# Optimization experiments

Measured on AMD Instinct MI355X. Metric: run time of the kernel, lower is better.

Reference implementation:

```python
import jax, jax.numpy as jnp
import numpy as np
from jax import lax

# dims
B, T, C, V, L = 4, 1024, 1024, 32000, 2
NR, NT, E = 6, 2, 8          # rwkv experts, transformer experts, total
HID = 4 * C                  # FFN hidden
P, R = 8, 64                 # bridge prefix_len, low_rank_dim
NH, HD = 16, 64              # heads, head_size


def _layernorm(x, g, b, eps=1e-5):
    m = jnp.mean(x, axis=-1, keepdims=True)
    v = jnp.var(x, axis=-1, keepdims=True)
    return (x - m) * lax.rsqrt(v + eps) * g + b


def setup_inputs() -> dict:
    key = jax.random.key(0)
    ks = list(jax.random.split(key, 32))
    it = iter(ks)
    def nrm(shape, s=0.02):
        return jax.random.normal(next(it), shape, dtype=jnp.float32) * s
    inp = {}
    inp['idx'] = jax.random.randint(next(it), (B, T), 0, V)
    inp['capital_shares'] = jax.random.uniform(next(it), (L, E), dtype=jnp.float32)
    inp['emb'] = nrm((V, C), 1.0)
    inp['head'] = nrm((C, V))
    inp['ln1_g'] = jnp.ones((L, C), jnp.float32)
    inp['ln1_b'] = jnp.zeros((L, C), jnp.float32)
    inp['ln2_g'] = jnp.ones((L, C), jnp.float32)
    inp['ln2_b'] = jnp.zeros((L, C), jnp.float32)
    inp['lno_g'] = jnp.ones((C,), jnp.float32)
    inp['lno_b'] = jnp.zeros((C,), jnp.float32)
    inp['att_Wr'] = nrm((L, C, C))
    inp['att_Wk'] = nrm((L, C, C))
    inp['att_Wv'] = nrm((L, C, C))
    inp['att_Wo'] = nrm((L, C, C))
    inp['att_decay'] = nrm((L, C), 1.0)
    inp['critic_wd'] = nrm((L, C))
    inp['critic_Wa'] = nrm((L, C, E))
    inp['bridge_Wdown'] = nrm((C, R))
    inp['bridge_Wup'] = nrm((P, R, C))
    inp['eWk'] = nrm((L, NR, C, HID))
    inp['eWv'] = nrm((L, NR, HID, C))
    inp['conf_r'] = nrm((L, NR, C))
    inp['tWq'] = nrm((L, NT, C, C))
    inp['tWk'] = nrm((L, NT, C, C))
    inp['tWv'] = nrm((L, NT, C, C))
    inp['tWo'] = nrm((L, NT, C, C))
    inp['conf_t'] = nrm((L, NT, C))
    return inp


def _forward(idx, capital_shares, emb, head, ln1_g, ln1_b, ln2_g, ln2_b,
             lno_g, lno_b, att_Wr, att_Wk, att_Wv, att_Wo, att_decay,
             critic_wd, critic_Wa, bridge_Wdown, bridge_Wup,
             eWk, eWv, conf_r, tWq, tWk, tWv, tWo, conf_t):
    x = emb[idx]                                   # [B,T,C]
    v_first = jnp.zeros_like(x)
    for l in range(L):
        # --- TimeMix (simplified RWKV: per-channel decayed kv state) ---
        x_ln = _layernorm(x, ln1_g[l], ln1_b[l])
        r = jax.nn.sigmoid(x_ln @ att_Wr[l])       # [B,T,C]
        k = x_ln @ att_Wk[l]
        v = x_ln @ att_Wv[l]
        if l == 0:
            v_first = v
        else:
            v = 0.5 * (v + v_first)
        w = jax.nn.sigmoid(att_decay[l])           # [C] decay in (0,1)
        def step(s, kv):
            kt, vt = kv
            s = w * s + kt * vt
            return s, s
        kT = jnp.swapaxes(k, 0, 1)                 # [T,B,C]
        vT = jnp.swapaxes(v, 0, 1)
        _, s_seq = lax.scan(step, jnp.zeros((B, C), x.dtype), (kT, vT))
        rwkv_state = jnp.swapaxes(s_seq, 0, 1)     # [B,T,C]
        att_out = (r * rwkv_state) @ att_Wo[l]
        x = x + att_out
        # --- routing (market) ---
        h = _layernorm(x, ln2_g[l], ln2_b[l])
        conf_rw = jax.nn.sigmoid(jnp.einsum('btc,ec->bte', h, conf_r[l]))
        conf_tr = jax.nn.sigmoid(jnp.einsum('btc,ec->bte', h, conf_t[l]))
        confidences = jnp.concatenate([conf_rw, conf_tr], axis=-1)  # [B,T,E]
        difficulty = jax.nn.softplus(jnp.einsum('btc,c->bt', h, critic_wd[l]))[..., None]
        affinity = jnp.einsum('btc,ce->bte', h, critic_Wa[l])
        subsidy = jnp.tanh(affinity)               # critic.apply_to_bids(0, affinity)
        bids = confidences * capital_shares[l] * difficulty + subsidy
        top2_vals, winners = lax.top_k(bids, 2)    # [B,T,2]
        weights = jax.nn.softmax(top2_vals, axis=-1)
        gate = (weights[..., 0:1] * jax.nn.one_hot(winners[..., 0], E, dtype=h.dtype)
                + weights[..., 1:2] * jax.nn.one_hot(winners[..., 1], E, dtype=h.dtype))  # [B,T,E]
        # --- bridge prefix (low-rank, shared) ---
        flat_h = h.reshape(-1, C)
        flat_state = rwkv_state.reshape(-1, C)
        u = (flat_h + flat_state) @ bridge_Wdown   # [N,R]
        prefix = jnp.einsum('nr,prc->npc', u, bridge_Wup)  # [N,P,C]
        # --- experts: dense-equivalent of gather/compute/scatter ---
        final = jnp.zeros_like(h)
        for e in range(NR):                        # squared-relu FFN experts
            hid = jnp.square(jax.nn.relu(h @ eWk[l, e]))
            final = final + gate[..., e:e + 1] * (hid @ eWv[l, e])
        scale = 1.0 / jnp.sqrt(jnp.float32(HD))
        for j in range(NT):                        # linear transformer experts over prefix
            q = (flat_h @ tWq[l, j]).reshape(-1, NH, HD)
            kp = (prefix @ tWk[l, j]).reshape(-1, P, NH, HD)
            vp = (prefix @ tWv[l, j]).reshape(-1, P, NH, HD)
            attn = jax.nn.softmax(jnp.einsum('nhd,nphd->nhp', q, kp) * scale, axis=-1)
            o = jnp.einsum('nhp,nphd->nhd', attn, vp).reshape(-1, C) @ tWo[l, j]
            final = final + gate[..., NR + j:NR + j + 1] * o.reshape(B, T, C)
        x = x + final
    x = _layernorm(x, lno_g, lno_b)
    return x @ head                                # [B,T,V] logits


def reference(idx, capital_shares, emb, head, ln1_g, ln1_b, ln2_g, ln2_b,
              lno_g, lno_b, att_Wr, att_Wk, att_Wv, att_Wo, att_decay,
              critic_wd, critic_Wa, bridge_Wdown, bridge_Wup,
              eWk, eWv, conf_r, tWq, tWk, tWv, tWo, conf_t):
    return _forward(idx, capital_shares, emb, head, ln1_g, ln1_b, ln2_g, ln2_b,
                    lno_g, lno_b, att_Wr, att_Wk, att_Wv, att_Wo, att_decay,
                    critic_wd, critic_Wa, bridge_Wdown, bridge_Wup,
                    eWk, eWv, conf_r, tWq, tWk, tWv, tWo, conf_t)
```

## Files before the change

### kernel.cpp

```cpp
#include <hip/hip_runtime.h>

typedef _Float16 h16;
typedef __attribute__((ext_vector_type(8))) _Float16 h16x8;
typedef __attribute__((ext_vector_type(4))) _Float16 h16x4;
typedef __attribute__((ext_vector_type(4))) float f32x4;

#define DEVFN static __device__ __forceinline__

DEVFN void gl_lds16(const void* g, void* l) {
  __builtin_amdgcn_global_load_lds((const __attribute__((address_space(1))) unsigned int*)g,
                                   (__attribute__((address_space(3))) unsigned int*)l, 16, 0, 0);
}
DEVFN void fsplit(float v, h16& hi, h16& lo) { hi = (h16)v; lo = (h16)(v - (float)hi); }
DEVFN float wred(float v) {
  #pragma unroll
  for (int m = 32; m >= 1; m >>= 1) v += __shfl_xor(v, m, 64);
  return v;
}
DEVFN float sigm(float x) { return 1.0f / (1.0f + expf(-x)); }
DEVFN float softpl(float x) { return fmaxf(x, 0.0f) + log1pf(expf(-fabsf(x))); }

enum { EPI_WRITE = 0, EPI_ADD = 1, EPI_SQRELU = 3, EPI_TSPLIT = 4, EPI_SCATTER = 5 };

template<bool SPLIT, int EPI, int MODE>
__global__ __launch_bounds__(256, 2) void gemm_k(
    const h16* __restrict__ Ah, const h16* __restrict__ Al, long lda, long sAz,
    const h16* __restrict__ Bh, const h16* __restrict__ Bl, long ldb, long sBz,
    float* __restrict__ C, long ldc, long sCz,
    h16* __restrict__ Oh, h16* __restrict__ Ol, long ldo,
    int K, int nmask, const float* __restrict__ rs, int rsStride,
    const int4* __restrict__ meta, int metaStep,
    const int* __restrict__ lists, int listStep,
    const int* __restrict__ mmap)
{
  __shared__ h16 As[(SPLIT ? 2 : 1) * 4096];
  __shared__ h16 Bs[(SPLIT ? 2 : 1) * 4096];
  const int tid = threadIdx.x;
  const int lane = tid & 63, wave = tid >> 6;
  const int wr = wave >> 1, wc = wave & 1;
  const long z = blockIdx.z;
  const long m0 = (long)blockIdx.x * 128, n0 = (long)blockIdx.y * 128;

  int cntv = 0, eIdx = 0, eOff = 0;
  long koff = 0;
  const int* lst = nullptr;
  if (MODE == 1) {
    const int4 mt = meta[z * metaStep];
    if ((int)m0 >= mt.y) return;
    cntv = mt.x; lst = lists + z * listStep;
  } else if (MODE == 2) {
    const int4 mt = meta[0];
    if ((int)m0 >= mt.y) return;
    cntv = mt.x; lst = lists; koff = z * (long)K;
  } else if (MODE == 3 || MODE == 4) {
    if ((int)m0 >= meta[8].x) return;
    eIdx = mmap[blockIdx.x];
    const int4 mt = meta[eIdx];
    cntv = mt.x; eOff = mt.z;
    lst = lists + eIdx * listStep;
    if (MODE == 4) koff = z * (long)K;
  }

  const long zb = (MODE == 3 || MODE == 4) ? (long)eIdx : z;
  const h16* pAh = Ah + z * sAz;
  const h16* pBh = Bh + zb * sBz;
  const h16* pAl = SPLIT ? (Al + z * sAz) : nullptr;
  const h16* pBl = SPLIT ? (Bl + zb * sBz) : nullptr;
  const int rA = wave * 16 + (lane >> 2);
  const int khalf = (lane & 3) * 8;
  long arow0, arow1;
  if (MODE == 1)      { arow0 = lst[m0 + rA]; arow1 = lst[m0 + rA + 64]; }
  else if (MODE == 3) { arow0 = lst[m0 + rA - eOff]; arow1 = lst[m0 + rA + 64 - eOff]; }
  else                { arow0 = m0 + rA; arow1 = arow0 + 64; }
  const long aoff0 = arow0 * lda + khalf + koff;
  const long aoff1 = arow1 * lda + khalf + koff;
  const long boff = (n0 + rA) * ldb + khalf + koff;
  h16* lA = &As[wave * 512];
  h16* lB = &Bs[wave * 512];
  const int fr = lane & 15, fq = lane >> 4;

  const f32x4 zero = {0.f, 0.f, 0.f, 0.f};
  f32x4 acc[4][4];
  #pragma unroll
  for (int m = 0; m < 4; m++)
    #pragma unroll
    for (int n = 0; n < 4; n++) acc[m][n] = zero;

  for (int k0 = 0; k0 < K; k0 += 32) {
    gl_lds16(pAh + aoff0 + k0, lA);
    gl_lds16(pAh + aoff1 + k0, lA + 2048);
    gl_lds16(pBh + boff + k0, lB);
    gl_lds16(pBh + boff + k0 + 64 * ldb, lB + 2048);
    if (SPLIT) {
      gl_lds16(pAl + aoff0 + k0, lA + 4096);
      gl_lds16(pAl + aoff1 + k0, lA + 4096 + 2048);
      gl_lds16(pBl + boff + k0, lB + 4096);
      gl_lds16(pBl + boff + k0 + 64 * ldb, lB + 4096 + 2048);
    }
    __syncthreads();
    h16x8 af[4], bf[4], afl[4], bfl[4];
    #pragma unroll
    for (int m = 0; m < 4; m++) {
      const int r = (wr * 64 + m * 16 + fr) * 32 + fq * 8;
      af[m] = *(const h16x8*)&As[r];
      if (SPLIT) afl[m] = *(const h16x8*)&As[4096 + r];
    }
    #pragma unroll
    for (int n = 0; n < 4; n++) {
      const int r = (wc * 64 + n * 16 + fr) * 32 + fq * 8;
      bf[n] = *(const h16x8*)&Bs[r];
      if (SPLIT) bfl[n] = *(const h16x8*)&Bs[4096 + r];
    }
    #pragma unroll
    for (int m = 0; m < 4; m++)
      #pragma unroll
      for (int n = 0; n < 4; n++) {
        acc[m][n] = __builtin_amdgcn_mfma_f32_16x16x32_f16(af[m], bf[n], acc[m][n], 0, 0, 0);
        if (SPLIT) {
          acc[m][n] = __builtin_amdgcn_mfma_f32_16x16x32_f16(af[m], bfl[n], acc[m][n], 0, 0, 0);
          acc[m][n] = __builtin_amdgcn_mfma_f32_16x16x32_f16(afl[m], bf[n], acc[m][n], 0, 0, 0);
        }
      }
    __syncthreads();
  }

  #pragma unroll
  for (int m = 0; m < 4; m++) {
    const long lrow = m0 + wr * 64 + m * 16 + fq * 4;
    #pragma unroll
    for (int n = 0; n < 4; n++) {
      const long gcol = n0 + wc * 64 + n * 16 + fr;
      if (nmask && gcol >= nmask) continue;
      if (EPI == EPI_TSPLIT) {
        h16x4 hv, lv;
        #pragma unroll
        for (int i = 0; i < 4; i++) { h16 a, b2; fsplit(acc[m][n][i], a, b2); hv[i] = a; lv[i] = b2; }
        *(h16x4*)&Oh[gcol * ldo + lrow] = hv;
        *(h16x4*)&Ol[gcol * ldo + lrow] = lv;
      } else if (EPI == EPI_SQRELU) {
        #pragma unroll
        for (int i = 0; i < 4; i++) {
          float v = acc[m][n][i];
          v = v > 0.f ? v * v : 0.f;
          const h16 a = (h16)v;
          Oh[(lrow + i) * ldo + gcol] = a;
          if (Ol) Ol[(lrow + i) * ldo + gcol] = (h16)(v - (float)a);
        }
      } else if (EPI == EPI_SCATTER) {
        #pragma unroll
        for (int i = 0; i < 4; i++) {
          const int slot = (int)lrow + i - eOff;
          if (slot >= cntv) continue;
          const int tok = lst[slot];
          const float g = rs[(long)tok * rsStride + (MODE == 4 ? eIdx : 0)];
          atomicAdd(&C[(long)tok * ldc + gcol], g * acc[m][n][i]);
        }
      } else {
        float* cp = C + z * sCz + lrow * ldc + gcol;
        #pragma unroll
        for (int i = 0; i < 4; i++) {
          const float v = acc[m][n][i];
          if (EPI == EPI_WRITE) cp[i * ldc] = v;
          else cp[i * ldc] += v;
        }
      }
    }
  }
}

template<bool LO>
__global__ __launch_bounds__(256) void k_tsplit(
    const float* __restrict__ in, long inZ,
    h16* __restrict__ oh, h16* __restrict__ ol, long outZ, int Kd, int Nd)
{
  __shared__ float t[64][65];
  const long z = blockIdx.z;
  in += z * inZ; oh += z * outZ; if (LO) ol += z * outZ;
  const int n0 = blockIdx.x * 64, k0 = blockIdx.y * 64;
  const int tr = threadIdx.x >> 4, tc = threadIdx.x & 15;
  #pragma unroll
  for (int r = 0; r < 4; r++) {
    const int row = r * 16 + tr;
    const float4 v = *(const float4*)&in[(long)(k0 + row) * Nd + n0 + tc * 4];
    t[row][tc * 4 + 0] = v.x; t[row][tc * 4 + 1] = v.y;
    t[row][tc * 4 + 2] = v.z; t[row][tc * 4 + 3] = v.w;
  }
  __syncthreads();
  #pragma unroll
  for (int r = 0; r < 4; r++) {
    const int nrow = r * 16 + tr;
    h16x4 hv, lv;
    #pragma unroll
    for (int i = 0; i < 4; i++) {
      h16 a, b2; fsplit(t[tc * 4 + i][nrow], a, b2);
      hv[i] = a; lv[i] = b2;
    }
    *(h16x4*)&oh[(long)(n0 + nrow) * Kd + k0 + tc * 4] = hv;
    if (LO) *(h16x4*)&ol[(long)(n0 + nrow) * Kd + k0 + tc * 4] = lv;
  }
}

__global__ void k_split(const float* __restrict__ in, h16* __restrict__ oh, h16* __restrict__ ol)
{
  const long i = (long)blockIdx.x * 256 + threadIdx.x;
  const float4 v = ((const float4*)in)[i];
  h16x4 hv, lv; h16 a, b2;
  fsplit(v.x, a, b2); hv[0] = a; lv[0] = b2;
  fsplit(v.y, a, b2); hv[1] = a; lv[1] = b2;
  fsplit(v.z, a, b2); hv[2] = a; lv[2] = b2;
  fsplit(v.w, a, b2); hv[3] = a; lv[3] = b2;
  ((h16x4*)oh)[i] = hv; ((h16x4*)ol)[i] = lv;
}

__global__ void k_embed(const int* __restrict__ idx, const float* __restrict__ emb, float* __restrict__ x)
{
  const int row = blockIdx.x;
  const long e = (long)idx[row] * 1024;
  ((float4*)(x + (long)row * 1024))[threadIdx.x] = ((const float4*)(emb + e))[threadIdx.x];
}

__global__ __launch_bounds__(256) void k_ln(
    const float* __restrict__ x, const float* __restrict__ g, const float* __restrict__ b,
    float* __restrict__ yf, h16* __restrict__ yh, h16* __restrict__ yl)
{
  const int row = blockIdx.x, tid = threadIdx.x;
  const float4 v = ((const float4*)(x + (long)row * 1024))[tid];
  __shared__ float red[4];
  const int wv = tid >> 6;
  float s = wred(v.x + v.y + v.z + v.w);
  if ((tid & 63) == 0) red[wv] = s;
  __syncthreads();
  const float mean = (red[0] + red[1] + red[2] + red[3]) * (1.0f / 1024.0f);
  const float d0 = v.x - mean, d1 = v.y - mean, d2 = v.z - mean, d3 = v.w - mean;
  float s2 = wred(d0 * d0 + d1 * d1 + d2 * d2 + d3 * d3);
  __syncthreads();
  if ((tid & 63) == 0) red[wv] = s2;
  __syncthreads();
  const float var = (red[0] + red[1] + red[2] + red[3]) * (1.0f / 1024.0f);
  const float rstd = 1.0f / sqrtf(var + 1e-5f);
  const float4 gv = ((const float4*)g)[tid];
  const float4 bv = ((const float4*)b)[tid];
  const float y0 = d0 * rstd * gv.x + bv.x;
  const float y1 = d1 * rstd * gv.y + bv.y;
  const float y2 = d2 * rstd * gv.z + bv.z;
  const float y3 = d3 * rstd * gv.w + bv.w;
  if (yf) { float4 o; o.x = y0; o.y = y1; o.z = y2; o.w = y3; ((float4*)(yf + (long)row * 1024))[tid] = o; }
  h16x4 hv, lv; h16 a, b2;
  fsplit(y0, a, b2); hv[0] = a; lv[0] = b2;
  fsplit(y1, a, b2); hv[1] = a; lv[1] = b2;
  fsplit(y2, a, b2); hv[2] = a; lv[2] = b2;
  fsplit(y3, a, b2); hv[3] = a; lv[3] = b2;
  *(h16x4*)(yh + (long)row * 1024 + tid * 4) = hv;
  if (yl) *(h16x4*)(yl + (long)row * 1024 + tid * 4) = lv;
}

__global__ void k_vfix(float* __restrict__ rkv, float* __restrict__ vfir, int mode)
{
  const int row = blockIdx.x, tid = threadIdx.x;
  float4* vp = (float4*)(rkv + (long)row * 3072 + 2048) + tid;
  float4* fp = (float4*)(vfir + (long)row * 1024) + tid;
  if (mode == 0) *fp = *vp;
  else {
    float4 a = *vp; const float4 b = *fp;
    a.x = 0.5f * (a.x + b.x); a.y = 0.5f * (a.y + b.y);
    a.z = 0.5f * (a.z + b.z); a.w = 0.5f * (a.w + b.w);
    *vp = a;
  }
}

__global__ __launch_bounds__(256) void k_scan1(const float* __restrict__ rkv,
                                               const float* __restrict__ dec, float* __restrict__ carry)
{
  const int gid = blockIdx.x * 256 + threadIdx.x;
  const int c = gid & 1023, bb = (gid >> 10) & 3, ch = gid >> 12;
  const float w = sigm(dec[c]);
  float s = 0.f;
  const long base = ((long)bb * 1024 + ch * 64) * 3072 + c;
  const float* kp_ = rkv + 1024 + base;
  const float* vp_ = rkv + 2048 + base;
  for (int t = 0; t < 64; t++) s = w * s + kp_[(long)t * 3072] * vp_[(long)t * 3072];
  carry[(ch * 4 + bb) * 1024 + c] = s;
}
__global__ void k_scan2(const float* __restrict__ dec, float* __restrict__ carry)
{
  const int gid = blockIdx.x * 256 + threadIdx.x;
  const int c = gid & 1023, bb = gid >> 10;
  const float w = sigm(dec[c]);
  float w64 = w;
  for (int i = 0; i < 6; i++) w64 *= w64;
  float s = 0.f;
  for (int j = 0; j < 16; j++) {
    const int o = (j * 4 + bb) * 1024 + c;
    const float a = carry[o];
    carry[o] = s;
    s = w64 * s + a;
  }
}
__global__ __launch_bounds__(256) void k_scan3(const float* __restrict__ rkv,
                                               const float* __restrict__ dec, const float* __restrict__ carry,
                                               float* __restrict__ st)
{
  const int gid = blockIdx.x * 256 + threadIdx.x;
  const int c = gid & 1023, bb = (gid >> 10) & 3, ch = gid >> 12;
  const float w = sigm(dec[c]);
  float s = carry[(ch * 4 + bb) * 1024 + c];
  const long base = ((long)bb * 1024 + ch * 64) * 3072 + c;
  const float* kp_ = rkv + 1024 + base;
  const float* vp_ = rkv + 2048 + base;
  float* so = st + ((long)bb * 1024 + ch * 64) * 1024 + c;
  for (int t = 0; t < 64; t++) {
    s = w * s + kp_[(long)t * 3072] * vp_[(long)t * 3072];
    so[(long)t * 1024] = s;
  }
}

__global__ void k_attin(const float* __restrict__ rkv, const float* __restrict__ s,
                        h16* __restrict__ oh, h16* __restrict__ ol)
{
  const int row = blockIdx.x, tid = threadIdx.x;
  const float4 rv = *((const float4*)(rkv + (long)row * 3072) + tid);
  const float4 sv = *((const float4*)(s + (long)row * 1024) + tid);
  h16x4 hv, lv; h16 a, b2;
  fsplit(sv.x * sigm(rv.x), a, b2); hv[0] = a; lv[0] = b2;
  fsplit(sv.y * sigm(rv.y), a, b2); hv[1] = a; lv[1] = b2;
  fsplit(sv.z * sigm(rv.z), a, b2); hv[2] = a; lv[2] = b2;
  fsplit(sv.w * sigm(rv.w), a, b2); hv[3] = a; lv[3] = b2;
  const long i = (long)row * 256 + tid;
  ((h16x4*)oh)[i] = hv; ((h16x4*)ol)[i] = lv;
}

__global__ void k_addsplit(const float* __restrict__ p, const float* __restrict__ q,
                           h16* __restrict__ oh, h16* __restrict__ ol)
{
  const long i = (long)blockIdx.x * 256 + threadIdx.x;
  const float4 av = ((const float4*)p)[i];
  const float4 bv = ((const float4*)q)[i];
  h16x4 hv, lv; h16 a, b2;
  fsplit(av.x + bv.x, a, b2); hv[0] = a; lv[0] = b2;
  fsplit(av.y + bv.y, a, b2); hv[1] = a; lv[1] = b2;
  fsplit(av.z + bv.z, a, b2); hv[2] = a; lv[2] = b2;
  fsplit(av.w + bv.w, a, b2); hv[3] = a; lv[3] = b2;
  ((h16x4*)oh)[i] = hv; ((h16x4*)ol)[i] = lv;
}

__global__ __launch_bounds__(256) void k_route(
    const float* __restrict__ h, const float* __restrict__ cr, const float* __restrict__ ct,
    const float* __restrict__ wd, const float* __restrict__ wa,
    const float* __restrict__ cap, float* __restrict__ gate)
{
  const int wv = threadIdx.x >> 6, ln = threadIdx.x & 63;
  const int row = blockIdx.x * 4 + wv;
  const float* hr = h + (long)row * 1024;
  float hreg[16];
  #pragma unroll
  for (int i = 0; i < 4; i++) {
    const float4 t = ((const float4*)hr)[ln * 4 + i];
    hreg[i * 4 + 0] = t.x; hreg[i * 4 + 1] = t.y; hreg[i * 4 + 2] = t.z; hreg[i * 4 + 3] = t.w;
  }
  float dots[17];
  #pragma unroll
  for (int e = 0; e < 6; e++) {
    float p = 0.f;
    #pragma unroll
    for (int j = 0; j < 16; j++) p += hreg[j] * cr[e * 1024 + ln * 16 + j];
    dots[e] = p;
  }
  #pragma unroll
  for (int e = 0; e < 2; e++) {
    float p = 0.f;
    #pragma unroll
    for (int j = 0; j < 16; j++) p += hreg[j] * ct[e * 1024 + ln * 16 + j];
    dots[6 + e] = p;
  }
  {
    float p = 0.f;
    #pragma unroll
    for (int j = 0; j < 16; j++) p += hreg[j] * wd[ln * 16 + j];
    dots[8] = p;
  }
  #pragma unroll
  for (int e = 0; e < 8; e++) {
    float p = 0.f;
    #pragma unroll
    for (int j = 0; j < 16; j++) p += hreg[j] * wa[(ln * 16 + j) * 8 + e];
    dots[9 + e] = p;
  }
  #pragma unroll
  for (int d = 0; d < 17; d++) dots[d] = wred(dots[d]);
  if (ln == 0) {
    float bids[8];
    const float diff = softpl(dots[8]);
    #pragma unroll
    for (int e = 0; e < 6; e++) bids[e] = sigm(dots[e]) * cap[e] * diff + tanhf(dots[9 + e]);
    #pragma unroll
    for (int e = 0; e < 2; e++) bids[6 + e] = sigm(dots[6 + e]) * cap[6 + e] * diff + tanhf(dots[15 + e]);
    int w0 = 0;
    for (int e = 1; e < 8; e++) if (bids[e] > bids[w0]) w0 = e;
    int w1 = -1;
    for (int e = 0; e < 8; e++) if (e != w0 && (w1 < 0 || bids[e] > bids[w1])) w1 = e;
    const float e1 = expf(bids[w1] - bids[w0]);
    const float q0 = 1.0f / (1.0f + e1), q1 = e1 / (1.0f + e1);
    for (int e = 0; e < 8; e++) gate[(long)row * 8 + e] = (e == w0) ? q0 : ((e == w1) ? q1 : 0.0f);
  }
}

__global__ void k_build(const float* __restrict__ gate, int* __restrict__ cnt, int* __restrict__ lists)
{
  const int t = blockIdx.x * 256 + threadIdx.x;
  #pragma unroll
  for (int e = 0; e < 8; e++)
    if (gate[(long)t * 8 + e] > 0.f) { const int s = atomicAdd(&cnt[e], 1); lists[e * 4224 + s] = t; }
}
__global__ void k_meta(const int* __restrict__ cnt, int4* __restrict__ meta, int* __restrict__ lists,
                       int* __restrict__ mmap)
{
  __shared__ int sc[8], sp[8], so[8];
  if (threadIdx.x == 0) {
    int acc = 0;
    for (int e = 0; e < 8; e++) {
      const int c = cnt[e], p = (c + 127) & ~127;
      sc[e] = c; sp[e] = p; so[e] = (e < 6) ? acc : 0;
      if (e < 6) acc += p;
    }
    meta[8] = make_int4(acc, acc >> 7, 0, 0);
    for (int b = 0; b < 128; b++) mmap[b] = 0;
    for (int e = 0; e < 6; e++)
      for (int b = so[e] >> 7; b < (so[e] + sp[e]) >> 7; b++) mmap[b] = e;
  }
  __syncthreads();
  const int e = threadIdx.x >> 5, i = threadIdx.x & 31;
  for (int s = sc[e] + i; s < sp[e]; s += 32) lists[e * 4224 + s] = 0;
  if (i == 0) meta[e] = make_int4(sc[e], sp[e], so[e], 0);
}

__global__ __launch_bounds__(256) void k_scores(const float* __restrict__ q, const float* __restrict__ kp,
                                                float* __restrict__ attn, const int4* __restrict__ meta)
{
  const int gw = blockIdx.x * 4 + (threadIdx.x >> 6), ln = threadIdx.x & 63;
  const int n = gw >> 4, hh = gw & 15;
  if (n >= meta->y) return;
  const float qv = q[(long)n * 1024 + hh * 64 + ln];
  float s[8];
  #pragma unroll
  for (int p = 0; p < 8; p++) {
    float t = qv * kp[(long)n * 8192 + p * 1024 + hh * 64 + ln];
    s[p] = wred(t) * 0.125f;
  }
  if (ln == 0) {
    float mx = s[0];
    #pragma unroll
    for (int p = 1; p < 8; p++) mx = fmaxf(mx, s[p]);
    float ex[8], sum = 0.f;
    #pragma unroll
    for (int p = 0; p < 8; p++) { ex[p] = expf(s[p] - mx); sum += ex[p]; }
    const float inv = 1.0f / sum;
    #pragma unroll
    for (int p = 0; p < 8; p++) attn[(long)n * 128 + hh * 8 + p] = ex[p] * inv;
  }
}

__global__ void k_omix(const float* __restrict__ attn, const float* __restrict__ vp,
                       h16* __restrict__ oh, h16* __restrict__ ol, const int4* __restrict__ meta)
{
  const long gid = (long)blockIdx.x * 256 + threadIdx.x;
  const int n = gid >> 10, hd = gid & 1023, hh = hd >> 6;
  if (n >= meta->y) return;
  const float* a = attn + (long)n * 128 + hh * 8;
  float o = 0.f;
  #pragma unroll
  for (int p = 0; p < 8; p++) o += a[p] * vp[(long)n * 8192 + p * 1024 + hd];
  h16 hi, lo; fsplit(o, hi, lo);
  oh[gid] = hi; ol[gid] = lo;
}

#define GEMM3(SPL, EPI, MODE, GRID, ...) do { \
  if (SPL) gemm_k<true,  EPI, MODE><<<GRID, 256, 0, stream>>>(__VA_ARGS__); \
  else     gemm_k<false, EPI, MODE><<<GRID, 256, 0, stream>>>(__VA_ARGS__); } while (0)

extern "C" void kernel_launch(void* const* d_in, const int* in_sizes, int n_in,
                              void* d_out, int out_size, void* d_ws, size_t ws_size,
                              hipStream_t stream)
{
  (void)in_sizes; (void)n_in; (void)out_size; (void)ws_size;
  const int*   idx   = (const int*)  d_in[0];
  const float* cap   = (const float*)d_in[1];
  const float* emb   = (const float*)d_in[2];
  const float* headw = (const float*)d_in[3];
  const float* ln1g  = (const float*)d_in[4];
  const float* ln1b  = (const float*)d_in[5];
  const float* ln2g  = (const float*)d_in[6];
  const float* ln2b  = (const float*)d_in[7];
  const float* lnog  = (const float*)d_in[8];
  const float* lnob  = (const float*)d_in[9];
  const float* aWr   = (const float*)d_in[10];
  const float* aWk   = (const float*)d_in[11];
  const float* aWv   = (const float*)d_in[12];
  const float* aWo   = (const float*)d_in[13];
  const float* adec  = (const float*)d_in[14];
  const float* cwd   = (const float*)d_in[15];
  const float* cWa   = (const float*)d_in[16];
  const float* bWd   = (const float*)d_in[17];
  const float* bWu   = (const float*)d_in[18];
  const float* eWkw  = (const float*)d_in[19];
  const float* eWvw  = (const float*)d_in[20];
  const float* confr = (const float*)d_in[21];
  const float* tWq   = (const float*)d_in[22];
  const float* tWkk  = (const float*)d_in[23];
  const float* tWv   = (const float*)d_in[24];
  const float* tWo   = (const float*)d_in[25];
  const float* conft = (const float*)d_in[26];
  float* out = (float*)d_out;

  char* ws = (char*)d_ws;
  size_t off = 0;
  auto alloc = [&](size_t n) -> char* {
    off = (off + 255) & ~(size_t)255;
    char* p = ws + off; off += n; return p;
  };
  const long M1 = 1048576, M4 = 4194304;

  h16* attWh = (h16*)alloc(8 * M1 * 2);
  h16* attWl = (h16*)alloc(8 * M1 * 2);
  h16* eWkh  = (h16*)alloc(12 * M4 * 2);
  h16* eWkl  = (h16*)alloc(6 * M4 * 2);
  h16* eWvh  = (h16*)alloc(12 * M4 * 2);
  h16* eWvl  = (h16*)alloc(6 * M4 * 2);
  h16* tWh   = (h16*)alloc(16 * M1 * 2);
  h16* tWl   = (h16*)alloc(8 * M1 * 2);
  h16* headh = (h16*)alloc(32768000ull * 2);
  h16* wdh   = (h16*)alloc(131072 * 2);
  h16* wdl   = (h16*)alloc(131072 * 2);
  h16* wuph  = (h16*)alloc(524288 * 2);
  h16* wupl  = (h16*)alloc(524288 * 2);
  h16* wukth = (h16*)alloc(524288 * 2);
  h16* wuktl = (h16*)alloc(524288 * 2);
  h16* wuvth = (h16*)alloc(524288 * 2);
  h16* wuvtl = (h16*)alloc(524288 * 2);
  h16* s1h   = (h16*)alloc(M4 * 2);
  h16* s1l   = (h16*)alloc(M4 * 2);
  h16* hh_   = (h16*)alloc(M4 * 2);
  h16* hl_   = (h16*)alloc(M4 * 2);
  h16* uh    = (h16*)alloc(262144 * 2);
  h16* ul    = (h16*)alloc(262144 * 2);
  float* x    = (float*)alloc(M4 * 4);
  float* vfir = (float*)alloc(M4 * 4);
  float* rkv  = (float*)alloc(3 * M4 * 4);
  float* st   = (float*)alloc(M4 * 4);
  float* hf   = (float*)alloc(M4 * 4);
  float* qf   = (float*)alloc(M4 * 4);
  char* big   = alloc(167772160);
  h16* hidh   = (h16*)big;
  h16* hidl   = (h16*)(big + 78643200ull);
  float* kp   = (float*)big;
  float* carry = (float*)alloc(65536 * 4);
  float* gate  = (float*)alloc(32768 * 4);
  float* uf    = (float*)alloc(262144 * 4);
  float* attn  = (float*)alloc(524288 * 4);
  int*   cnt8  = (int*)alloc(32);
  int4*  metaA = (int4*)alloc(16 * 16);
  int*   lists = (int*)alloc(8 * 4224 * 4);
  int*   mmap  = (int*)alloc(128 * 4);

  const float* aW[4] = {aWr, aWk, aWv, aWo};
  for (int w = 0; w < 4; w++)
    k_tsplit<true><<<dim3(16, 16, 2), 256, 0, stream>>>(aW[w], M1, attWh + w * M1, attWl + w * M1, 4 * M1, 1024, 1024);
  k_tsplit<true ><<<dim3(64, 16, 6), 256, 0, stream>>>(eWkw, M4, eWkh, eWkl, M4, 1024, 4096);
  k_tsplit<false><<<dim3(64, 16, 6), 256, 0, stream>>>(eWkw + 6 * M4, M4, eWkh + 6 * M4, nullptr, M4, 1024, 4096);
  k_tsplit<true ><<<dim3(16, 64, 6), 256, 0, stream>>>(eWvw, M4, eWvh, eWvl, M4, 4096, 1024);
  k_tsplit<false><<<dim3(16, 64, 6), 256, 0, stream>>>(eWvw + 6 * M4, M4, eWvh + 6 * M4, nullptr, M4, 4096, 1024);
  const float* tWsrc[4] = {tWq, tWkk, tWv, tWo};
  for (int m = 0; m < 4; m++) {
    k_tsplit<true ><<<dim3(16, 16, 2), 256, 0, stream>>>(tWsrc[m], M1, tWh + m * M1, tWl + m * M1, 4 * M1, 1024, 1024);
    k_tsplit<false><<<dim3(16, 16, 2), 256, 0, stream>>>(tWsrc[m] + 2 * M1, M1, tWh + (8 + m) * M1, nullptr, 4 * M1, 1024, 1024);
  }
  k_tsplit<false><<<dim3(500, 16, 1), 256, 0, stream>>>(headw, 0, headh, nullptr, 0, 1024, 32000);
  k_tsplit<true ><<<dim3(1, 16, 1), 256, 0, stream>>>(bWd, 0, wdh, wdl, 0, 1024, 64);
  hipMemsetAsync(wdh + 65536, 0, 65536 * 2, stream);
  hipMemsetAsync(wdl + 65536, 0, 65536 * 2, stream);
  k_split<<<512, 256, 0, stream>>>(bWu, wuph, wupl);

  k_embed<<<4096, 256, 0, stream>>>(idx, emb, x);

  for (int l = 0; l < 2; l++) {
    const bool SE = (l == 0);
    k_ln<<<4096, 256, 0, stream>>>(x, ln1g + l * 1024, ln1b + l * 1024, nullptr, s1h, s1l);
    GEMM3(true, EPI_WRITE, 0, dim3(32, 24),
          s1h, s1l, 1024, 0, attWh + (l * 4) * M1, attWl + (l * 4) * M1, 1024, 0,
          rkv, 3072, 0, nullptr, nullptr, 0, 1024, 0, nullptr, 0, nullptr, 0, nullptr, 0, nullptr);
    k_vfix<<<4096, 256, 0, stream>>>(rkv, vfir, l == 0 ? 0 : 1);
    k_scan1<<<256, 256, 0, stream>>>(rkv, adec + l * 1024, carry);
    k_scan2<<<16, 256, 0, stream>>>(adec + l * 1024, carry);
    k_scan3<<<256, 256, 0, stream>>>(rkv, adec + l * 1024, carry, st);
    k_attin<<<4096, 256, 0, stream>>>(rkv, st, s1h, s1l);
    GEMM3(true, EPI_ADD, 0, dim3(32, 8),
          s1h, s1l, 1024, 0, attWh + (l * 4 + 3) * M1, attWl + (l * 4 + 3) * M1, 1024, 0,
          x, 1024, 0, nullptr, nullptr, 0, 1024, 0, nullptr, 0, nullptr, 0, nullptr, 0, nullptr);
    k_ln<<<4096, 256, 0, stream>>>(x, ln2g + l * 1024, ln2b + l * 1024, hf, hh_, hl_);
    k_route<<<1024, 256, 0, stream>>>(hf, confr + l * 6144, conft + l * 2048, cwd + l * 1024, cWa + l * 8192, cap + l * 8, gate);
    hipMemsetAsync(cnt8, 0, 32, stream);
    k_build<<<16, 256, 0, stream>>>(gate, cnt8, lists);
    k_meta<<<1, 256, 0, stream>>>(cnt8, metaA, lists, mmap);
    k_addsplit<<<4096, 256, 0, stream>>>(hf, st, s1h, s1l);
    GEMM3(true, EPI_WRITE, 0, dim3(32, 1),
          s1h, s1l, 1024, 0, wdh, wdl, 1024, 0,
          uf, 64, 0, nullptr, nullptr, 0, 1024, 64, nullptr, 0, nullptr, 0, nullptr, 0, nullptr);
    k_split<<<256, 256, 0, stream>>>(uf, uh, ul);
    GEMM3(SE, EPI_SQRELU, 3, dim3(70, 32),
          hh_, hl_, 1024, 0, eWkh + l * 6 * M4, eWkl, 1024, M4,
          nullptr, 0, 0, hidh, SE ? hidl : nullptr, 4096, 1024, 0, nullptr, 0, metaA, 1, lists, 4224, mmap);
    GEMM3(SE, EPI_SCATTER, 4, dim3(70, 8, 4),
          hidh, hidl, 4096, 0, eWvh + l * 6 * M4, eWvl, 4096, M4,
          x, 1024, 0, nullptr, nullptr, 0, 1024, 0, gate, 8, metaA, 1, lists, 4224, mmap);
    for (int j = 0; j < 2; j++) {
      const long wi = (l * 2 + j) * 4, wl = j * 4;
      const int4* mt = metaA + 6 + j;
      const int* lstT = lists + (6 + j) * 4224;
      GEMM3(SE, EPI_TSPLIT, 0, dim3(4, 8),
            wuph, wupl, 1024, 0, tWh + (wi + 1) * M1, tWl + (wl + 1) * M1, 1024, 0,
            nullptr, 0, 0, wukth, wuktl, 512, 1024, 0, nullptr, 0, nullptr, 0, nullptr, 0, nullptr);
      GEMM3(SE, EPI_TSPLIT, 0, dim3(4, 8),
            wuph, wupl, 1024, 0, tWh + (wi + 2) * M1, tWl + (wl + 2) * M1, 1024, 0,
            nullptr, 0, 0, wuvth, wuvtl, 512, 1024, 0, nullptr, 0, nullptr, 0, nullptr, 0, nullptr);
      GEMM3(SE, EPI_WRITE, 1, dim3(32, 8),
            hh_, hl_, 1024, 0, tWh + (wi + 0) * M1, tWl + (wl + 0) * M1, 1024, 0,
            qf, 1024, 0, nullptr, nullptr, 0, 1024, 0, nullptr, 0, mt, 0, lstT, 0, nullptr);
      GEMM3(SE, EPI_WRITE, 1, dim3(32, 8, 8),
            uh, ul, 64, 0, wukth, wuktl, 512, 64,
            kp, 8192, 1024, nullptr, nullptr, 0, 64, 0, nullptr, 0, mt, 0, lstT, 0, nullptr);
      k_scores<<<16384, 256, 0, stream>>>(qf, kp, attn, mt);
      GEMM3(SE, EPI_WRITE, 1, dim3(32, 8, 8),
            uh, ul, 64, 0, wuvth, wuvtl, 512, 64,
            kp, 8192, 1024, nullptr, nullptr, 0, 64, 0, nullptr, 0, mt, 0, lstT, 0, nullptr);
      k_omix<<<16384, 256, 0, stream>>>(attn, kp, s1h, s1l, mt);
      GEMM3(SE, EPI_SCATTER, 2, dim3(32, 8, 4),
            s1h, s1l, 1024, 0, tWh + (wi + 3) * M1, tWl + (wl + 3) * M1, 1024, 0,
            x, 1024, 0, nullptr, nullptr, 0, 256, 0, gate + 6 + j, 8, mt, 0, lstT, 0, nullptr);
    }
  }

  k_ln<<<4096, 256, 0, stream>>>(x, lnog, lnob, nullptr, s1h, s1l);
  GEMM3(false, EPI_WRITE, 0, dim3(32, 250),
        s1h, nullptr, 1024, 0, headh, nullptr, 1024, 0,
        out, 32000, 0, nullptr, nullptr, 0, 1024, 0, nullptr, 0, nullptr, 0, nullptr, 0, nullptr);
}
```

Before: 3.381 ms.

## Add 256x256-tile GEMM kernel for expert FFN and LM head

Adds a second GEMM kernel using 256x256 output tiles with 512 threads (8 waves, 8x4 MFMA accumulators each). The grouped expert FFN GEMMs (modes 3/4) and the final vocab-head GEMM move to it, and expert padding and block mapping in k_meta change from 128 to 256 rows. The larger tiles raise arithmetic intensity and cut repeated loads of A and B. In exchange, occupancy is limited to one block per CU with higher register and LDS pressure, more padded rows per expert, and fewer blocks for load balance.

```diff
diff --git a/kernel.cpp b/kernel.cpp
--- a/kernel.cpp
+++ b/kernel.cpp
@@ -30,8 +30,7 @@
     h16* __restrict__ Oh, h16* __restrict__ Ol, long ldo,
     int K, int nmask, const float* __restrict__ rs, int rsStride,
     const int4* __restrict__ meta, int metaStep,
-    const int* __restrict__ lists, int listStep,
-    const int* __restrict__ mmap)
+    const int* __restrict__ lists, int listStep)
 {
   __shared__ h16 As[(SPLIT ? 2 : 1) * 4096];
   __shared__ h16 Bs[(SPLIT ? 2 : 1) * 4096];
@@ -41,7 +40,7 @@
   const long z = blockIdx.z;
   const long m0 = (long)blockIdx.x * 128, n0 = (long)blockIdx.y * 128;
 
-  int cntv = 0, eIdx = 0, eOff = 0;
+  int cntv = 0;
   long koff = 0;
   const int* lst = nullptr;
   if (MODE == 1) {
@@ -52,26 +51,17 @@
     const int4 mt = meta[0];
     if ((int)m0 >= mt.y) return;
     cntv = mt.x; lst = lists; koff = z * (long)K;
-  } else if (MODE == 3 || MODE == 4) {
-    if ((int)m0 >= meta[8].x) return;
-    eIdx = mmap[blockIdx.x];
-    const int4 mt = meta[eIdx];
-    cntv = mt.x; eOff = mt.z;
-    lst = lists + eIdx * listStep;
-    if (MODE == 4) koff = z * (long)K;
-  }
-
-  const long zb = (MODE == 3 || MODE == 4) ? (long)eIdx : z;
+  }
+
   const h16* pAh = Ah + z * sAz;
-  const h16* pBh = Bh + zb * sBz;
+  const h16* pBh = Bh + z * sBz;
   const h16* pAl = SPLIT ? (Al + z * sAz) : nullptr;
-  const h16* pBl = SPLIT ? (Bl + zb * sBz) : nullptr;
+  const h16* pBl = SPLIT ? (Bl + z * sBz) : nullptr;
   const int rA = wave * 16 + (lane >> 2);
   const int khalf = (lane & 3) * 8;
   long arow0, arow1;
-  if (MODE == 1)      { arow0 = lst[m0 + rA]; arow1 = lst[m0 + rA + 64]; }
-  else if (MODE == 3) { arow0 = lst[m0 + rA - eOff]; arow1 = lst[m0 + rA + 64 - eOff]; }
-  else                { arow0 = m0 + rA; arow1 = arow0 + 64; }
+  if (MODE == 1) { arow0 = lst[m0 + rA]; arow1 = lst[m0 + rA + 64]; }
+  else           { arow0 = m0 + rA; arow1 = arow0 + 64; }
   const long aoff0 = arow0 * lda + khalf + koff;
   const long aoff1 = arow1 * lda + khalf + koff;
   const long boff = (n0 + rA) * ldb + khalf + koff;
@@ -137,7 +127,125 @@
         for (int i = 0; i < 4; i++) { h16 a, b2; fsplit(acc[m][n][i], a, b2); hv[i] = a; lv[i] = b2; }
         *(h16x4*)&Oh[gcol * ldo + lrow] = hv;
         *(h16x4*)&Ol[gcol * ldo + lrow] = lv;
-      } else if (EPI == EPI_SQRELU) {
+      } else if (EPI == EPI_SCATTER) {
+        #pragma unroll
+        for (int i = 0; i < 4; i++) {
+          const int slot = (int)lrow + i;
+          if (slot >= cntv) continue;
+          const int tok = lst[slot];
+          const float g = rs[(long)tok * rsStride];
+          atomicAdd(&C[(long)tok * ldc + gcol], g * acc[m][n][i]);
+        }
+      } else {
+        float* cp = C + z * sCz + lrow * ldc + gcol;
+        #pragma unroll
+        for (int i = 0; i < 4; i++) {
+          const float v = acc[m][n][i];
+          if (EPI == EPI_WRITE) cp[i * ldc] = v;
+          else cp[i * ldc] += v;
+        }
+      }
+    }
+  }
+}
+
+template<bool SPLIT, int EPI, int MODE>
+__global__ __launch_bounds__(512, 1) void gemm256_k(
+    const h16* __restrict__ Ah, const h16* __restrict__ Al, long lda,
+    const h16* __restrict__ Bh, const h16* __restrict__ Bl, long ldb, long sBz,
+    float* __restrict__ C, long ldc,
+    h16* __restrict__ Oh, h16* __restrict__ Ol, long ldo,
+    int K, const float* __restrict__ rs, int rsStride,
+    const int4* __restrict__ meta, const int* __restrict__ lists, int listStep,
+    const int* __restrict__ mmap)
+{
+  __shared__ h16 As[(SPLIT ? 2 : 1) * 8192];
+  __shared__ h16 Bs[(SPLIT ? 2 : 1) * 8192];
+  const int tid = threadIdx.x;
+  const int lane = tid & 63, wave = tid >> 6;
+  const int wr = wave >> 2, wc = wave & 3;
+  const long m0 = (long)blockIdx.x * 256, n0 = (long)blockIdx.y * 256;
+
+  int cntv = 0, eIdx = 0, eOff = 0;
+  long koff = 0;
+  const int* lst = nullptr;
+  if (MODE == 3 || MODE == 4) {
+    if ((int)m0 >= meta[8].x) return;
+    eIdx = mmap[blockIdx.x];
+    const int4 mt = meta[eIdx];
+    cntv = mt.x; eOff = mt.z;
+    lst = lists + eIdx * listStep;
+    if (MODE == 4) koff = blockIdx.z * (long)K;
+  }
+
+  const h16* pAh = Ah;
+  const h16* pBh = Bh + (long)eIdx * sBz;
+  const h16* pAl = SPLIT ? Al : nullptr;
+  const h16* pBl = SPLIT ? (Bl + (long)eIdx * sBz) : nullptr;
+  const int rA = (tid >> 2) & 127;
+  const int khalf = (lane & 3) * 8;
+  long arow0, arow1;
+  if (MODE == 3) { arow0 = lst[m0 + rA - eOff]; arow1 = lst[m0 + rA + 128 - eOff]; }
+  else           { arow0 = m0 + rA; arow1 = arow0 + 128; }
+  const long aoff0 = arow0 * lda + khalf + koff;
+  const long aoff1 = arow1 * lda + khalf + koff;
+  const long boff0 = (n0 + rA) * ldb + khalf + koff;
+  const long boff1 = boff0 + 128 * ldb;
+  h16* lA = &As[wave * 512];
+  h16* lB = &Bs[wave * 512];
+  const int fr = lane & 15, fq = lane >> 4;
+
+  const f32x4 zero = {0.f, 0.f, 0.f, 0.f};
+  f32x4 acc[8][4];
+  #pragma unroll
+  for (int m = 0; m < 8; m++)
+    #pragma unroll
+    for (int n = 0; n < 4; n++) acc[m][n] = zero;
+
+  for (int k0 = 0; k0 < K; k0 += 32) {
+    gl_lds16(pAh + aoff0 + k0, lA);
+    gl_lds16(pAh + aoff1 + k0, lA + 4096);
+    gl_lds16(pBh + boff0 + k0, lB);
+    gl_lds16(pBh + boff1 + k0, lB + 4096);
+    if (SPLIT) {
+      gl_lds16(pAl + aoff0 + k0, lA + 8192);
+      gl_lds16(pAl + aoff1 + k0, lA + 8192 + 4096);
+      gl_lds16(pBl + boff0 + k0, lB + 8192);
+      gl_lds16(pBl + boff1 + k0, lB + 8192 + 4096);
+    }
+    __syncthreads();
+    h16x8 bf[4], bfl[4];
+    #pragma unroll
+    for (int n = 0; n < 4; n++) {
+      const int r = (wc * 64 + n * 16 + fr) * 32 + fq * 8;
+      bf[n] = *(const h16x8*)&Bs[r];
+      if (SPLIT) bfl[n] = *(const h16x8*)&Bs[8192 + r];
+    }
+    #pragma unroll
+    for (int m = 0; m < 8; m++) {
+      const int r = (wr * 128 + m * 16 + fr) * 32 + fq * 8;
+      const h16x8 af = *(const h16x8*)&As[r];
+      h16x8 afl;
+      if (SPLIT) afl = *(const h16x8*)&As[8192 + r];
+      #pragma unroll
+      for (int n = 0; n < 4; n++) {
+        acc[m][n] = __builtin_amdgcn_mfma_f32_16x16x32_f16(af, bf[n], acc[m][n], 0, 0, 0);
+        if (SPLIT) {
+          acc[m][n] = __builtin_amdgcn_mfma_f32_16x16x32_f16(af, bfl[n], acc[m][n], 0, 0, 0);
+          acc[m][n] = __builtin_amdgcn_mfma_f32_16x16x32_f16(afl, bf[n], acc[m][n], 0, 0, 0);
+        }
+      }
+    }
+    __syncthreads();
+  }
+
+  #pragma unroll
+  for (int m = 0; m < 8; m++) {
+    const long lrow = m0 + wr * 128 + m * 16 + fq * 4;
+    #pragma unroll
+    for (int n = 0; n < 4; n++) {
+      const long gcol = n0 + wc * 64 + n * 16 + fr;
+      if (EPI == EPI_SQRELU) {
         #pragma unroll
         for (int i = 0; i < 4; i++) {
           float v = acc[m][n][i];
@@ -152,17 +260,12 @@
           const int slot = (int)lrow + i - eOff;
           if (slot >= cntv) continue;
           const int tok = lst[slot];
-          const float g = rs[(long)tok * rsStride + (MODE == 4 ? eIdx : 0)];
-          atomicAdd(&C[(long)tok * ldc + gcol], g * acc[m][n][i]);
+          atomicAdd(&C[(long)tok * ldc + gcol], rs[(long)tok * rsStride + eIdx] * acc[m][n][i]);
         }
       } else {
-        float* cp = C + z * sCz + lrow * ldc + gcol;
+        float* cp = C + lrow * ldc + gcol;
         #pragma unroll
-        for (int i = 0; i < 4; i++) {
-          const float v = acc[m][n][i];
-          if (EPI == EPI_WRITE) cp[i * ldc] = v;
-          else cp[i * ldc] += v;
-        }
+        for (int i = 0; i < 4; i++) cp[i * ldc] = acc[m][n][i];
       }
     }
   }
@@ -418,14 +521,14 @@
   if (threadIdx.x == 0) {
     int acc = 0;
     for (int e = 0; e < 8; e++) {
-      const int c = cnt[e], p = (c + 127) & ~127;
+      const int c = cnt[e], p = (c + 255) & ~255;
       sc[e] = c; sp[e] = p; so[e] = (e < 6) ? acc : 0;
       if (e < 6) acc += p;
     }
-    meta[8] = make_int4(acc, acc >> 7, 0, 0);
-    for (int b = 0; b < 128; b++) mmap[b] = 0;
+    meta[8] = make_int4(acc, 0, 0, 0);
+    for (int b = 0; b < 64; b++) mmap[b] = 0;
     for (int e = 0; e < 6; e++)
-      for (int b = so[e] >> 7; b < (so[e] + sp[e]) >> 7; b++) mmap[b] = e;
+      for (int b = so[e] >> 8; b < (so[e] + sp[e]) >> 8; b++) mmap[b] = e;
   }
   __syncthreads();
   const int e = threadIdx.x >> 5, i = threadIdx.x & 31;
@@ -476,6 +579,9 @@
 #define GEMM3(SPL, EPI, MODE, GRID, ...) do { \
   if (SPL) gemm_k<true,  EPI, MODE><<<GRID, 256, 0, stream>>>(__VA_ARGS__); \
   else     gemm_k<false, EPI, MODE><<<GRID, 256, 0, stream>>>(__VA_ARGS__); } while (0)
+#define GEMM256(SPL, EPI, MODE, GRID, ...) do { \
+  if (SPL) gemm256_k<true,  EPI, MODE><<<GRID, 512, 0, stream>>>(__VA_ARGS__); \
+  else     gemm256_k<false, EPI, MODE><<<GRID, 512, 0, stream>>>(__VA_ARGS__); } while (0)
 
 extern "C" void kernel_launch(void* const* d_in, const int* in_sizes, int n_in,
                               void* d_out, int out_size, void* d_ws, size_t ws_size,
@@ -550,7 +656,7 @@
   float* qf   = (float*)alloc(M4 * 4);
   char* big   = alloc(167772160);
   h16* hidh   = (h16*)big;
-  h16* hidl   = (h16*)(big + 78643200ull);
+  h16* hidl   = (h16*)(big + 83886080ull);
   float* kp   = (float*)big;
   float* carry = (float*)alloc(65536 * 4);
   float* gate  = (float*)alloc(32768 * 4);
@@ -559,7 +665,7 @@
   int*   cnt8  = (int*)alloc(32);
   int4*  metaA = (int4*)alloc(16 * 16);
   int*   lists = (int*)alloc(8 * 4224 * 4);
-  int*   mmap  = (int*)alloc(128 * 4);
+  int*   mmap  = (int*)alloc(64 * 4);
 
   const float* aW[4] = {aWr, aWk, aWv, aWo};
   for (int w = 0; w < 4; w++)
@@ -586,7 +692,7 @@
     k_ln<<<4096, 256, 0, stream>>>(x, ln1g + l * 1024, ln1b + l * 1024, nullptr, s1h, s1l);
     GEMM3(true, EPI_WRITE, 0, dim3(32, 24),
           s1h, s1l, 1024, 0, attWh + (l * 4) * M1, attWl + (l * 4) * M1, 1024, 0,
-          rkv, 3072, 0, nullptr, nullptr, 0, 1024, 0, nullptr, 0, nullptr, 0, nullptr, 0, nullptr);
+          rkv, 3072, 0, nullptr, nullptr, 0, 1024, 0, nullptr, 0, nullptr, 0, nullptr, 0);
     k_vfix<<<4096, 256, 0, stream>>>(rkv, vfir, l == 0 ? 0 : 1);
     k_scan1<<<256, 256, 0, stream>>>(rkv, adec + l * 1024, carry);
     k_scan2<<<16, 256, 0, stream>>>(adec + l * 1024, carry);
@@ -594,7 +700,7 @@
     k_attin<<<4096, 256, 0, stream>>>(rkv, st, s1h, s1l);
     GEMM3(true, EPI_ADD, 0, dim3(32, 8),
           s1h, s1l, 1024, 0, attWh + (l * 4 + 3) * M1, attWl + (l * 4 + 3) * M1, 1024, 0,
-          x, 1024, 0, nullptr, nullptr, 0, 1024, 0, nullptr, 0, nullptr, 0, nullptr, 0, nullptr);
+          x, 1024, 0, nullptr, nullptr, 0, 1024, 0, nullptr, 0, nullptr, 0, nullptr, 0);
     k_ln<<<4096, 256, 0, stream>>>(x, ln2g + l * 1024, ln2b + l * 1024, hf, hh_, hl_);
     k_route<<<1024, 256, 0, stream>>>(hf, confr + l * 6144, conft + l * 2048, cwd + l * 1024, cWa + l * 8192, cap + l * 8, gate);
     hipMemsetAsync(cnt8, 0, 32, stream);
@@ -603,43 +709,46 @@
     k_addsplit<<<4096, 256, 0, stream>>>(hf, st, s1h, s1l);
     GEMM3(true, EPI_WRITE, 0, dim3(32, 1),
           s1h, s1l, 1024, 0, wdh, wdl, 1024, 0,
-          uf, 64, 0, nullptr, nullptr, 0, 1024, 64, nullptr, 0, nullptr, 0, nullptr, 0, nullptr);
+          uf, 64, 0, nullptr, nullptr, 0, 1024, 64, nullptr, 0, nullptr, 0, nullptr, 0);
     k_split<<<256, 256, 0, stream>>>(uf, uh, ul);
-    GEMM3(SE, EPI_SQRELU, 3, dim3(70, 32),
-          hh_, hl_, 1024, 0, eWkh + l * 6 * M4, eWkl, 1024, M4,
-          nullptr, 0, 0, hidh, SE ? hidl : nullptr, 4096, 1024, 0, nullptr, 0, metaA, 1, lists, 4224, mmap);
-    GEMM3(SE, EPI_SCATTER, 4, dim3(70, 8, 4),
-          hidh, hidl, 4096, 0, eWvh + l * 6 * M4, eWvl, 4096, M4,
-          x, 1024, 0, nullptr, nullptr, 0, 1024, 0, gate, 8, metaA, 1, lists, 4224, mmap);
+    GEMM256(SE, EPI_SQRELU, 3, dim3(40, 16),
+            hh_, hl_, 1024, eWkh + l * 6 * M4, eWkl, 1024, M4,
+            nullptr, 0, hidh, SE ? hidl : nullptr, 4096,
+            1024, nullptr, 0, metaA, lists, 4224, mmap);
+    GEMM256(SE, EPI_SCATTER, 4, dim3(40, 4, 4),
+            hidh, hidl, 4096, eWvh + l * 6 * M4, eWvl, 4096, M4,
+            x, 1024, nullptr, nullptr, 0,
+            1024, gate, 8, metaA, lists, 4224, mmap);
     for (int j = 0; j < 2; j++) {
       const long wi = (l * 2 + j) * 4, wl = j * 4;
       const int4* mt = metaA + 6 + j;
       const int* lstT = lists + (6 + j) * 4224;
       GEMM3(SE, EPI_TSPLIT, 0, dim3(4, 8),
             wuph, wupl, 1024, 0, tWh + (wi + 1) * M1, tWl + (wl + 1) * M1, 1024, 0,
-            nullptr, 0, 0, wukth, wuktl, 512, 1024, 0, nullptr, 0, nullptr, 0, nullptr, 0, nullptr);
+            nullptr, 0, 0, wukth, wuktl, 512, 1024, 0, nullptr, 0, nullptr, 0, nullptr, 0);
       GEMM3(SE, EPI_TSPLIT, 0, dim3(4, 8),
             wuph, wupl, 1024, 0, tWh + (wi + 2) * M1, tWl + (wl + 2) * M1, 1024, 0,
-            nullptr, 0, 0, wuvth, wuvtl, 512, 1024, 0, nullptr, 0, nullptr, 0, nullptr, 0, nullptr);
+            nullptr, 0, 0, wuvth, wuvtl, 512, 1024, 0, nullptr, 0, nullptr, 0, nullptr, 0);
       GEMM3(SE, EPI_WRITE, 1, dim3(32, 8),
             hh_, hl_, 1024, 0, tWh + (wi + 0) * M1, tWl + (wl + 0) * M1, 1024, 0,
-            qf, 1024, 0, nullptr, nullptr, 0, 1024, 0, nullptr, 0, mt, 0, lstT, 0, nullptr);
+            qf, 1024, 0, nullptr, nullptr, 0, 1024, 0, nullptr, 0, mt, 0, lstT, 0);
       GEMM3(SE, EPI_WRITE, 1, dim3(32, 8, 8),
             uh, ul, 64, 0, wukth, wuktl, 512, 64,
-            kp, 8192, 1024, nullptr, nullptr, 0, 64, 0, nullptr, 0, mt, 0, lstT, 0, nullptr);
+            kp, 8192, 1024, nullptr, nullptr, 0, 64, 0, nullptr, 0, mt, 0, lstT, 0);
       k_scores<<<16384, 256, 0, stream>>>(qf, kp, attn, mt);
       GEMM3(SE, EPI_WRITE, 1, dim3(32, 8, 8),
             uh, ul, 64, 0, wuvth, wuvtl, 512, 64,
-            kp, 8192, 1024, nullptr, nullptr, 0, 64, 0, nullptr, 0, mt, 0, lstT, 0, nullptr);
+            kp, 8192, 1024, nullptr, nullptr, 0, 64, 0, nullptr, 0, mt, 0, lstT, 0);
       k_omix<<<16384, 256, 0, stream>>>(attn, kp, s1h, s1l, mt);
       GEMM3(SE, EPI_SCATTER, 2, dim3(32, 8, 4),
             s1h, s1l, 1024, 0, tWh + (wi + 3) * M1, tWl + (wl + 3) * M1, 1024, 0,
-            x, 1024, 0, nullptr, nullptr, 0, 256, 0, gate + 6 + j, 8, mt, 0, lstT, 0, nullptr);
+            x, 1024, 0, nullptr, nullptr, 0, 256, 0, gate + 6 + j, 8, mt, 0, lstT, 0);
     }
   }
 
   k_ln<<<4096, 256, 0, stream>>>(x, lnog, lnob, nullptr, s1h, s1l);
-  GEMM3(false, EPI_WRITE, 0, dim3(32, 250),
-        s1h, nullptr, 1024, 0, headh, nullptr, 1024, 0,
-        out, 32000, 0, nullptr, nullptr, 0, 1024, 0, nullptr, 0, nullptr, 0, nullptr, 0, nullptr);
-}
+  GEMM256(false, EPI_WRITE, 0, dim3(16, 125),
+          s1h, nullptr, 1024, headh, nullptr, 1024, 0,
+          out, 32000, nullptr, nullptr, 0,
+          1024, nullptr, 0, nullptr, nullptr, 0, nullptr);
+}
```

Result: slower. 3.457 ms (+2.3%).
